# Performance work log

Measured on AMD Instinct MI355X. Metric: run time of the kernel, lower is better.

Reference implementation:

```python
import jax, jax.numpy as jnp
import numpy as np

N = 65536          # nodes
E = N * 7          # edges (avg_degree = n_edge_type = 7)
C_IN = 128
C_OUT = 128
N_EDGE_TYPE = 7
N_NODE_TYPE = 5
FEAT = C_IN + N_NODE_TYPE  # 133, channels after one-hot concat


def setup_inputs() -> dict:
    key = jax.random.key(0)
    k1, k2, k3, k4, k5 = jax.random.split(key, 5)
    x = jax.random.normal(k1, (N, C_IN), dtype=jnp.float32)
    edge_idx = jax.random.randint(k2, (2, E), 0, N, dtype=jnp.int64)
    edge_type = jax.random.randint(k3, (E,), 0, N_EDGE_TYPE, dtype=jnp.int64)
    node_type = jax.random.randint(k4, (N,), 0, N_NODE_TYPE, dtype=jnp.int64)
    # uniform init a la module's reset_parameters
    fan_in = 7 * C_IN
    fan_out = 7 * C_OUT
    a = np.sqrt(3.0) * np.sqrt(2.0 / (fan_in + fan_out))
    weights = jax.random.uniform(k5, (N_EDGE_TYPE * FEAT, C_OUT), dtype=jnp.float32,
                                 minval=-a, maxval=a)
    return {"x": x, "edge_idx": edge_idx, "edge_type": edge_type,
            "node_type": node_type, "weights": weights}


def reference(x, edge_idx, edge_type, node_type, weights):
    # one-hot node type concat (n_node_type > 1 branch)
    one_hot = jax.nn.one_hot(node_type, N_NODE_TYPE, dtype=x.dtype)
    xa = jnp.concatenate([x, one_hot], axis=1)          # [N, FEAT]
    row, col = edge_idx[0], edge_idx[1]
    seg = row * N_EDGE_TYPE + edge_type                 # [E]
    gathered = xa[col]                                  # [E, FEAT]
    num_seg = N * N_EDGE_TYPE
    sums = jax.ops.segment_sum(gathered, seg, num_segments=num_seg)
    cnt = jax.ops.segment_sum(jnp.ones((E,), dtype=xa.dtype), seg, num_segments=num_seg)
    col_data = sums / jnp.maximum(cnt, 1.0)[:, None]    # scatter_mean
    # overwrite self-loop slot (last edge type) with node's own features
    self_idx = jnp.arange(N, dtype=jnp.int64) * N_EDGE_TYPE + (N_EDGE_TYPE - 1)
    col_data = col_data.at[self_idx].set(xa)
    out = col_data.reshape(N, N_EDGE_TYPE * FEAT) @ weights  # [N, C_OUT]
    return out
```

## Files before the change

### kernel.cpp

```cpp
#include <hip/hip_runtime.h>
#include <hip/hip_bf16.h>

#define N_NODES 65536
#define N_EDGES (N_NODES * 7)
#define NSEG    (N_NODES * 7)
#define CAP     12
#define ZROW    65536

typedef short short8 __attribute__((ext_vector_type(8)));
typedef float f32x4  __attribute__((ext_vector_type(4)));

__device__ __forceinline__ unsigned short f2bf(float f) {
    return __builtin_bit_cast(unsigned short, (__bf16)f);
}
__device__ __forceinline__ unsigned pack2(float lo, float hi) {
    return (unsigned)f2bf(lo) | ((unsigned)f2bf(hi) << 16);
}
__device__ __forceinline__ float bflo(unsigned d) { return __uint_as_float(d << 16); }
__device__ __forceinline__ float bfhi(unsigned d) { return __uint_as_float(d & 0xffff0000u); }

__global__ __launch_bounds__(256) void k_big(const float* __restrict__ x,
                                             const int* __restrict__ eidx,
                                             const int* __restrict__ etype,
                                             const int* __restrict__ ntype,
                                             const float* __restrict__ W,
                                             unsigned short* __restrict__ xb,
                                             unsigned short* __restrict__ wb,
                                             unsigned* __restrict__ seg32,
                                             unsigned short* __restrict__ scol) {
    int i = blockIdx.x * 256 + threadIdx.x;

    if (i < N_EDGES) {
        int t = etype[i];
        if (t < 6) {
            int r = eidx[i];
            int c = eidx[N_EDGES + i];
            int u = ntype[c];
            unsigned seg = (unsigned)r * 7u + (unsigned)t;
            unsigned inc = 1u | (1u << (7 + 5 * u));
            unsigned old = atomicAdd(&seg32[seg], inc);
            unsigned slot = old & 0x7fu;
            if (slot < CAP) scol[seg * CAP + slot] = (unsigned short)c;
        }
    }

    {
        int row = i >> 4, mm = i & 15;
        const f32x4* p = reinterpret_cast<const f32x4*>(x + (size_t)row * 128 + mm * 8);
        f32x4 v0 = p[0], v1 = p[1];
        uint4 w;
        w.x = pack2(v0[0], v0[1]); w.y = pack2(v0[2], v0[3]);
        w.z = pack2(v1[0], v1[1]); w.w = pack2(v1[2], v1[3]);
        reinterpret_cast<uint4*>(xb)[i] = w;
    }

    if (i < 16) reinterpret_cast<uint4*>(xb + (size_t)ZROW * 128)[i] = (uint4){0u, 0u, 0u, 0u};

    if (i < 143360) {
        int j    = i & 7;
        int lane = (i >> 3) & 63;
        int cb   = (i >> 9) & 7;
        int tkc  = i >> 12;
        int kc   = tkc % 5;
        int t    = tkc / 5;
        int k = kc * 32 + ((lane >> 4) << 3) + j;
        int c = cb * 16 + (lane & 15);
        float v = (k < 133) ? W[(t * 133 + k) * 128 + c] : 0.0f;
        wb[i] = f2bf(v);
    }
}

__global__ __launch_bounds__(512, 4) void k_main(const unsigned short* __restrict__ xb,
                                                 const int* __restrict__ ntype,
                                                 const unsigned* __restrict__ seg32,
                                                 const unsigned short* __restrict__ scol,
                                                 const unsigned short* __restrict__ wb,
                                                 float* __restrict__ out) {
    __shared__ unsigned short sA[7 * 32 * 168];

    const int tid  = threadIdx.x;
    const int lane = tid & 63;
    const int wid  = tid >> 6;
    const int n0   = blockIdx.x * 32;
    const int r    = tid >> 4;
    const int m    = tid & 15;
    const int n    = n0 + r;

    for (int i = tid; i < 7 * 32 * 12; i += 512) {
        int row = i / 12, j = i - row * 12;
        reinterpret_cast<unsigned*>(sA)[row * 84 + 68 + j] = 0u;
    }

    unsigned sv[6], c_t[6];
    uint2 q2[6];
    #pragma unroll
    for (int t = 0; t < 6; ++t) {
        sv[t]  = seg32[n * 7 + t];
        c_t[t] = sv[t] & 0x7fu;
        q2[t]  = *reinterpret_cast<const uint2*>(scol + ((size_t)n * 7 + t) * CAP);
    }

    short8 xA[6], xB[6], xS;
    #pragma unroll
    for (int t = 0; t < 6; ++t) {
        unsigned cA = (c_t[t] >= 1u) ? (q2[t].x & 0xffffu) : (unsigned)ZROW;
        unsigned cB = (c_t[t] >= 2u) ? (q2[t].x >> 16)     : (unsigned)ZROW;
        xA[t] = *reinterpret_cast<const short8*>(xb + (size_t)cA * 128 + m * 8);
        xB[t] = *reinterpret_cast<const short8*>(xb + (size_t)cB * 128 + m * 8);
    }
    xS = *reinterpret_cast<const short8*>(xb + (size_t)n * 128 + m * 8);
    const int ntS = ntype[n];

    #pragma unroll
    for (int t = 0; t < 6; ++t) {
        const unsigned cntv = c_t[t];
        const float inv = (cntv > 1u) ? __builtin_amdgcn_rcpf((float)cntv) : 1.0f;

        uint4 a4 = *reinterpret_cast<const uint4*>(&xA[t]);
        uint4 b4 = *reinterpret_cast<const uint4*>(&xB[t]);
        float a[8];
        a[0] = bflo(a4.x) + bflo(b4.x); a[1] = bfhi(a4.x) + bfhi(b4.x);
        a[2] = bflo(a4.y) + bflo(b4.y); a[3] = bfhi(a4.y) + bfhi(b4.y);
        a[4] = bflo(a4.z) + bflo(b4.z); a[5] = bfhi(a4.z) + bfhi(b4.z);
        a[6] = bflo(a4.w) + bflo(b4.w); a[7] = bfhi(a4.w) + bfhi(b4.w);

        if (cntv >= 3u) {
            const unsigned ce = (cntv < (unsigned)CAP) ? cntv : (unsigned)CAP;
            {
                unsigned c2 = q2[t].y & 0xffffu;
                short8 v = *reinterpret_cast<const short8*>(xb + (size_t)c2 * 128 + m * 8);
                uint4 v4 = *reinterpret_cast<const uint4*>(&v);
                a[0] += bflo(v4.x); a[1] += bfhi(v4.x);
                a[2] += bflo(v4.y); a[3] += bfhi(v4.y);
                a[4] += bflo(v4.z); a[5] += bfhi(v4.z);
                a[6] += bflo(v4.w); a[7] += bfhi(v4.w);
            }
            if (ce >= 4u) {
                unsigned c3 = q2[t].y >> 16;
                short8 v = *reinterpret_cast<const short8*>(xb + (size_t)c3 * 128 + m * 8);
                uint4 v4 = *reinterpret_cast<const uint4*>(&v);
                a[0] += bflo(v4.x); a[1] += bfhi(v4.x);
                a[2] += bflo(v4.y); a[3] += bfhi(v4.y);
                a[4] += bflo(v4.z); a[5] += bfhi(v4.z);
                a[6] += bflo(v4.w); a[7] += bfhi(v4.w);
                const size_t segbase = ((size_t)n * 7 + t) * CAP;
                for (unsigned e = 4; e < ce; ++e) {
                    unsigned c = scol[segbase + e];
                    short8 ve = *reinterpret_cast<const short8*>(xb + (size_t)c * 128 + m * 8);
                    uint4 v4e = *reinterpret_cast<const uint4*>(&ve);
                    a[0] += bflo(v4e.x); a[1] += bfhi(v4e.x);
                    a[2] += bflo(v4e.y); a[3] += bfhi(v4e.y);
                    a[4] += bflo(v4e.z); a[5] += bfhi(v4e.z);
                    a[6] += bflo(v4e.w); a[7] += bfhi(v4e.w);
                }
            }
        }

        uint4 w;
        w.x = pack2(a[0] * inv, a[1] * inv); w.y = pack2(a[2] * inv, a[3] * inv);
        w.z = pack2(a[4] * inv, a[5] * inv); w.w = pack2(a[6] * inv, a[7] * inv);
        *reinterpret_cast<uint4*>(sA + (t * 32 + r) * 168 + m * 8) = w;

        if (m < 4) {
            int i0 = 2 * m, i1 = 2 * m + 1;
            float g0 = (i0 < 5) ? (float)((sv[t] >> (7 + 5 * i0)) & 31u) : 0.f;
            float g1 = (i1 < 5) ? (float)((sv[t] >> (7 + 5 * i1)) & 31u) : 0.f;
            reinterpret_cast<unsigned*>(sA)[(t * 32 + r) * 84 + 64 + m] =
                pack2(g0 * inv, g1 * inv);
        }
    }

    *reinterpret_cast<uint4*>(sA + (6 * 32 + r) * 168 + m * 8) =
        *reinterpret_cast<const uint4*>(&xS);
    if (m < 4) {
        float g0 = (ntS == 2 * m) ? 1.f : 0.f;
        float g1 = (ntS == 2 * m + 1) ? 1.f : 0.f;
        reinterpret_cast<unsigned*>(sA)[(6 * 32 + r) * 84 + 64 + m] = pack2(g0, g1);
    }

    short8 bv[2][5];
    #pragma unroll
    for (int kc = 0; kc < 5; ++kc)
        bv[0][kc] = *reinterpret_cast<const short8*>(
            wb + (((kc * 8 + wid) << 6) + lane) * 8);

    __syncthreads();

    f32x4 acc0 = {0.f, 0.f, 0.f, 0.f};
    f32x4 acc1 = {0.f, 0.f, 0.f, 0.f};
    const int ar = lane & 15;
    const int hi = (lane >> 4) << 3;

    #pragma unroll
    for (int t = 0; t < 7; ++t) {
        const int cur = t & 1, nxt = cur ^ 1;
        if (t < 6) {
            #pragma unroll
            for (int kc = 0; kc < 5; ++kc)
                bv[nxt][kc] = *reinterpret_cast<const short8*>(
                    wb + (((((t + 1) * 5 + kc) * 8 + wid) << 6) + lane) * 8);
        }
        #pragma unroll
        for (int kc = 0; kc < 5; ++kc) {
            short8 a0 = *reinterpret_cast<const short8*>(
                sA + (t * 32 + ar) * 168 + kc * 32 + hi);
            short8 a1 = *reinterpret_cast<const short8*>(
                sA + (t * 32 + 16 + ar) * 168 + kc * 32 + hi);
            acc0 = __builtin_amdgcn_mfma_f32_16x16x32_bf16(a0, bv[cur][kc], acc0, 0, 0, 0);
            acc1 = __builtin_amdgcn_mfma_f32_16x16x32_bf16(a1, bv[cur][kc], acc1, 0, 0, 0);
        }
    }

    const int orow = n0 + ((lane >> 4) << 2);
    const int ocol = (wid << 4) + (lane & 15);
    #pragma unroll
    for (int rr = 0; rr < 4; ++rr) {
        out[(size_t)(orow + rr) * 128 + ocol]      = acc0[rr];
        out[(size_t)(orow + 16 + rr) * 128 + ocol] = acc1[rr];
    }
}


extern "C" void kernel_launch(void* const* d_in, const int* in_sizes, int n_in,
                              void* d_out, int out_size, void* d_ws, size_t ws_size,
                              hipStream_t stream) {
    const float* x     = (const float*)d_in[0];
    const int*   eidx  = (const int*)d_in[1];
    const int*   etype = (const int*)d_in[2];
    const int*   ntype = (const int*)d_in[3];
    const float* W     = (const float*)d_in[4];
    float* out = (float*)d_out;

    unsigned short* xb    = (unsigned short*)d_ws;
    unsigned short* wb    = (unsigned short*)((char*)d_ws + 16777472);
    unsigned*       seg32 = (unsigned*)((char*)d_ws + 17064192);
    unsigned short* scol  = (unsigned short*)((char*)d_ws + 18899200);

    hipMemsetAsync(seg32, 0, NSEG * sizeof(unsigned), stream);
    k_big <<<4096,         256, 0, stream>>>(x, eidx, etype, ntype, W, xb, wb, seg32, scol);
    k_main<<<N_NODES / 32, 512, 0, stream>>>(xb, ntype, seg32, scol, wb, out);
}
```

Before: 81.44 us.

## Replace LDS-staged 8-wave block with single-wave 32x32 MFMA fused gather-GEMM

The main kernel changes from a 512-thread block that gathers neighbour means into shared memory and then runs 16x16x32 MFMAs to a single 64-lane wave per 32 nodes. That wave gathers its A fragments straight into registers and feeds them to 32x32x16 MFMAs over all 128 output columns, and the weight pre-pack layout is changed to match. This removes the shared memory, the barrier and the LDS round trip. In exchange each wave loops serially over edge types and streams the full weight matrix, so occupancy and latency hiding per CU drop and weight traffic per block grows.

```diff
diff --git a/kernel.cpp b/kernel.cpp
--- a/kernel.cpp
+++ b/kernel.cpp
@@ -9,6 +9,7 @@
 
 typedef short short8 __attribute__((ext_vector_type(8)));
 typedef float f32x4  __attribute__((ext_vector_type(4)));
+typedef float f32x16 __attribute__((ext_vector_type(16)));
 
 __device__ __forceinline__ unsigned short f2bf(float f) {
     return __builtin_bit_cast(unsigned short, (__bf16)f);
@@ -56,167 +57,133 @@
 
     if (i < 16) reinterpret_cast<uint4*>(xb + (size_t)ZROW * 128)[i] = (uint4){0u, 0u, 0u, 0u};
 
-    if (i < 143360) {
+    if (i < 129024) {
         int j    = i & 7;
         int lane = (i >> 3) & 63;
-        int cb   = (i >> 9) & 7;
-        int tkc  = i >> 12;
-        int kc   = tkc % 5;
-        int t    = tkc / 5;
-        int k = kc * 32 + ((lane >> 4) << 3) + j;
-        int c = cb * 16 + (lane & 15);
+        int cg   = (i >> 9) & 3;
+        int tkc  = i >> 11;
+        int kc   = tkc % 9;
+        int t    = tkc / 9;
+        int k = kc * 16 + ((lane >> 5) << 3) + j;
+        int c = (cg << 5) + (lane & 31);
         float v = (k < 133) ? W[(t * 133 + k) * 128 + c] : 0.0f;
         wb[i] = f2bf(v);
     }
 }
 
-__global__ __launch_bounds__(512, 4) void k_main(const unsigned short* __restrict__ xb,
-                                                 const int* __restrict__ ntype,
-                                                 const unsigned* __restrict__ seg32,
-                                                 const unsigned short* __restrict__ scol,
-                                                 const unsigned short* __restrict__ wb,
-                                                 float* __restrict__ out) {
-    __shared__ unsigned short sA[7 * 32 * 168];
-
-    const int tid  = threadIdx.x;
-    const int lane = tid & 63;
-    const int wid  = tid >> 6;
+__global__ __launch_bounds__(64, 4) void k_main(const unsigned short* __restrict__ xb,
+                                                const int* __restrict__ ntype,
+                                                const unsigned* __restrict__ seg32,
+                                                const unsigned short* __restrict__ scol,
+                                                const unsigned short* __restrict__ wb,
+                                                float* __restrict__ out) {
+    const int lane = threadIdx.x;
+    const int r    = lane & 31;
+    const int h    = lane >> 5;
     const int n0   = blockIdx.x * 32;
-    const int r    = tid >> 4;
-    const int m    = tid & 15;
     const int n    = n0 + r;
-
-    for (int i = tid; i < 7 * 32 * 12; i += 512) {
-        int row = i / 12, j = i - row * 12;
-        reinterpret_cast<unsigned*>(sA)[row * 84 + 68 + j] = 0u;
-    }
-
-    unsigned sv[6], c_t[6];
-    uint2 q2[6];
+    const int choff = h * 8;
+
+    const int ntS = ntype[n];
+
+    f32x16 acc[4];
     #pragma unroll
-    for (int t = 0; t < 6; ++t) {
-        sv[t]  = seg32[n * 7 + t];
-        c_t[t] = sv[t] & 0x7fu;
-        q2[t]  = *reinterpret_cast<const uint2*>(scol + ((size_t)n * 7 + t) * CAP);
-    }
-
-    short8 xA[6], xB[6], xS;
+    for (int cg = 0; cg < 4; ++cg)
+        #pragma unroll
+        for (int q = 0; q < 16; ++q) acc[cg][q] = 0.f;
+
+    #pragma unroll 1
+    for (int t = 0; t < 7; ++t) {
+        unsigned svt = 0, cnt, cA, cB;
+        uint2 q2t = {0u, 0u};
+        if (t < 6) {
+            svt = seg32[n * 7 + t];
+            cnt = svt & 0x7fu;
+            q2t = *reinterpret_cast<const uint2*>(scol + ((size_t)n * 7 + t) * CAP);
+            cA = (cnt >= 1u) ? (q2t.x & 0xffffu) : (unsigned)ZROW;
+            cB = (cnt >= 2u) ? (q2t.x >> 16)     : (unsigned)ZROW;
+        } else {
+            cnt = 1u; cA = (unsigned)n; cB = (unsigned)ZROW;
+        }
+        const float inv = (cnt > 1u) ? __builtin_amdgcn_rcpf((float)cnt) : 1.0f;
+        const unsigned ce = (cnt < (unsigned)CAP) ? cnt : (unsigned)CAP;
+        const size_t segbase = ((size_t)n * 7 + t) * CAP;
+
+        #pragma unroll
+        for (int kc = 0; kc < 8; ++kc) {
+            uint4 a4 = *reinterpret_cast<const uint4*>(
+                xb + (size_t)cA * 128 + kc * 16 + choff);
+            uint4 w;
+            if (cnt <= 1u) {
+                w = a4;
+            } else {
+                uint4 b4 = *reinterpret_cast<const uint4*>(
+                    xb + (size_t)cB * 128 + kc * 16 + choff);
+                float f[8];
+                f[0] = bflo(a4.x) + bflo(b4.x); f[1] = bfhi(a4.x) + bfhi(b4.x);
+                f[2] = bflo(a4.y) + bflo(b4.y); f[3] = bfhi(a4.y) + bfhi(b4.y);
+                f[4] = bflo(a4.z) + bflo(b4.z); f[5] = bfhi(a4.z) + bfhi(b4.z);
+                f[6] = bflo(a4.w) + bflo(b4.w); f[7] = bfhi(a4.w) + bfhi(b4.w);
+                if (cnt >= 3u) {
+                    for (unsigned e = 2; e < ce; ++e) {
+                        unsigned c = scol[segbase + e];
+                        uint4 v4 = *reinterpret_cast<const uint4*>(
+                            xb + (size_t)c * 128 + kc * 16 + choff);
+                        f[0] += bflo(v4.x); f[1] += bfhi(v4.x);
+                        f[2] += bflo(v4.y); f[3] += bfhi(v4.y);
+                        f[4] += bflo(v4.z); f[5] += bfhi(v4.z);
+                        f[6] += bflo(v4.w); f[7] += bfhi(v4.w);
+                    }
+                }
+                w.x = pack2(f[0] * inv, f[1] * inv);
+                w.y = pack2(f[2] * inv, f[3] * inv);
+                w.z = pack2(f[4] * inv, f[5] * inv);
+                w.w = pack2(f[6] * inv, f[7] * inv);
+            }
+            short8 av = *reinterpret_cast<const short8*>(&w);
+            #pragma unroll
+            for (int cg = 0; cg < 4; ++cg) {
+                short8 bv = *reinterpret_cast<const short8*>(
+                    wb + ((((t * 9 + kc) * 4 + cg) << 6) + lane) * 8);
+                acc[cg] = __builtin_amdgcn_mfma_f32_32x32x16_bf16(av, bv, acc[cg], 0, 0, 0);
+            }
+        }
+
+        {
+            uint4 w = {0u, 0u, 0u, 0u};
+            if (h == 0) {
+                float g0, g1, g2, g3, g4;
+                if (t < 6) {
+                    g0 = (float)((svt >> 7)  & 31u) * inv;
+                    g1 = (float)((svt >> 12) & 31u) * inv;
+                    g2 = (float)((svt >> 17) & 31u) * inv;
+                    g3 = (float)((svt >> 22) & 31u) * inv;
+                    g4 = (float)((svt >> 27) & 31u) * inv;
+                } else {
+                    g0 = (ntS == 0) ? 1.f : 0.f; g1 = (ntS == 1) ? 1.f : 0.f;
+                    g2 = (ntS == 2) ? 1.f : 0.f; g3 = (ntS == 3) ? 1.f : 0.f;
+                    g4 = (ntS == 4) ? 1.f : 0.f;
+                }
+                w.x = pack2(g0, g1); w.y = pack2(g2, g3); w.z = pack2(g4, 0.f);
+            }
+            short8 av = *reinterpret_cast<const short8*>(&w);
+            #pragma unroll
+            for (int cg = 0; cg < 4; ++cg) {
+                short8 bv = *reinterpret_cast<const short8*>(
+                    wb + ((((t * 9 + 8) * 4 + cg) << 6) + lane) * 8);
+                acc[cg] = __builtin_amdgcn_mfma_f32_32x32x16_bf16(av, bv, acc[cg], 0, 0, 0);
+            }
+        }
+    }
+
+    const int col = lane & 31;
     #pragma unroll
-    for (int t = 0; t < 6; ++t) {
-        unsigned cA = (c_t[t] >= 1u) ? (q2[t].x & 0xffffu) : (unsigned)ZROW;
-        unsigned cB = (c_t[t] >= 2u) ? (q2[t].x >> 16)     : (unsigned)ZROW;
-        xA[t] = *reinterpret_cast<const short8*>(xb + (size_t)cA * 128 + m * 8);
-        xB[t] = *reinterpret_cast<const short8*>(xb + (size_t)cB * 128 + m * 8);
-    }
-    xS = *reinterpret_cast<const short8*>(xb + (size_t)n * 128 + m * 8);
-    const int ntS = ntype[n];
-
-    #pragma unroll
-    for (int t = 0; t < 6; ++t) {
-        const unsigned cntv = c_t[t];
-        const float inv = (cntv > 1u) ? __builtin_amdgcn_rcpf((float)cntv) : 1.0f;
-
-        uint4 a4 = *reinterpret_cast<const uint4*>(&xA[t]);
-        uint4 b4 = *reinterpret_cast<const uint4*>(&xB[t]);
-        float a[8];
-        a[0] = bflo(a4.x) + bflo(b4.x); a[1] = bfhi(a4.x) + bfhi(b4.x);
-        a[2] = bflo(a4.y) + bflo(b4.y); a[3] = bfhi(a4.y) + bfhi(b4.y);
-        a[4] = bflo(a4.z) + bflo(b4.z); a[5] = bfhi(a4.z) + bfhi(b4.z);
-        a[6] = bflo(a4.w) + bflo(b4.w); a[7] = bfhi(a4.w) + bfhi(b4.w);
-
-        if (cntv >= 3u) {
-            const unsigned ce = (cntv < (unsigned)CAP) ? cntv : (unsigned)CAP;
-            {
-                unsigned c2 = q2[t].y & 0xffffu;
-                short8 v = *reinterpret_cast<const short8*>(xb + (size_t)c2 * 128 + m * 8);
-                uint4 v4 = *reinterpret_cast<const uint4*>(&v);
-                a[0] += bflo(v4.x); a[1] += bfhi(v4.x);
-                a[2] += bflo(v4.y); a[3] += bfhi(v4.y);
-                a[4] += bflo(v4.z); a[5] += bfhi(v4.z);
-                a[6] += bflo(v4.w); a[7] += bfhi(v4.w);
-            }
-            if (ce >= 4u) {
-                unsigned c3 = q2[t].y >> 16;
-                short8 v = *reinterpret_cast<const short8*>(xb + (size_t)c3 * 128 + m * 8);
-                uint4 v4 = *reinterpret_cast<const uint4*>(&v);
-                a[0] += bflo(v4.x); a[1] += bfhi(v4.x);
-                a[2] += bflo(v4.y); a[3] += bfhi(v4.y);
-                a[4] += bflo(v4.z); a[5] += bfhi(v4.z);
-                a[6] += bflo(v4.w); a[7] += bfhi(v4.w);
-                const size_t segbase = ((size_t)n * 7 + t) * CAP;
-                for (unsigned e = 4; e < ce; ++e) {
-                    unsigned c = scol[segbase + e];
-                    short8 ve = *reinterpret_cast<const short8*>(xb + (size_t)c * 128 + m * 8);
-                    uint4 v4e = *reinterpret_cast<const uint4*>(&ve);
-                    a[0] += bflo(v4e.x); a[1] += bfhi(v4e.x);
-                    a[2] += bflo(v4e.y); a[3] += bfhi(v4e.y);
-                    a[4] += bflo(v4e.z); a[5] += bfhi(v4e.z);
-                    a[6] += bflo(v4e.w); a[7] += bfhi(v4e.w);
-                }
-            }
-        }
-
-        uint4 w;
-        w.x = pack2(a[0] * inv, a[1] * inv); w.y = pack2(a[2] * inv, a[3] * inv);
-        w.z = pack2(a[4] * inv, a[5] * inv); w.w = pack2(a[6] * inv, a[7] * inv);
-        *reinterpret_cast<uint4*>(sA + (t * 32 + r) * 168 + m * 8) = w;
-
-        if (m < 4) {
-            int i0 = 2 * m, i1 = 2 * m + 1;
-            float g0 = (i0 < 5) ? (float)((sv[t] >> (7 + 5 * i0)) & 31u) : 0.f;
-            float g1 = (i1 < 5) ? (float)((sv[t] >> (7 + 5 * i1)) & 31u) : 0.f;
-            reinterpret_cast<unsigned*>(sA)[(t * 32 + r) * 84 + 64 + m] =
-                pack2(g0 * inv, g1 * inv);
-        }
-    }
-
-    *reinterpret_cast<uint4*>(sA + (6 * 32 + r) * 168 + m * 8) =
-        *reinterpret_cast<const uint4*>(&xS);
-    if (m < 4) {
-        float g0 = (ntS == 2 * m) ? 1.f : 0.f;
-        float g1 = (ntS == 2 * m + 1) ? 1.f : 0.f;
-        reinterpret_cast<unsigned*>(sA)[(6 * 32 + r) * 84 + 64 + m] = pack2(g0, g1);
-    }
-
-    short8 bv[2][5];
-    #pragma unroll
-    for (int kc = 0; kc < 5; ++kc)
-        bv[0][kc] = *reinterpret_cast<const short8*>(
-            wb + (((kc * 8 + wid) << 6) + lane) * 8);
-
-    __syncthreads();
-
-    f32x4 acc0 = {0.f, 0.f, 0.f, 0.f};
-    f32x4 acc1 = {0.f, 0.f, 0.f, 0.f};
-    const int ar = lane & 15;
-    const int hi = (lane >> 4) << 3;
-
-    #pragma unroll
-    for (int t = 0; t < 7; ++t) {
-        const int cur = t & 1, nxt = cur ^ 1;
-        if (t < 6) {
-            #pragma unroll
-            for (int kc = 0; kc < 5; ++kc)
-                bv[nxt][kc] = *reinterpret_cast<const short8*>(
-                    wb + (((((t + 1) * 5 + kc) * 8 + wid) << 6) + lane) * 8);
-        }
+    for (int cg = 0; cg < 4; ++cg) {
         #pragma unroll
-        for (int kc = 0; kc < 5; ++kc) {
-            short8 a0 = *reinterpret_cast<const short8*>(
-                sA + (t * 32 + ar) * 168 + kc * 32 + hi);
-            short8 a1 = *reinterpret_cast<const short8*>(
-                sA + (t * 32 + 16 + ar) * 168 + kc * 32 + hi);
-            acc0 = __builtin_amdgcn_mfma_f32_16x16x32_bf16(a0, bv[cur][kc], acc0, 0, 0, 0);
-            acc1 = __builtin_amdgcn_mfma_f32_16x16x32_bf16(a1, bv[cur][kc], acc1, 0, 0, 0);
-        }
-    }
-
-    const int orow = n0 + ((lane >> 4) << 2);
-    const int ocol = (wid << 4) + (lane & 15);
-    #pragma unroll
-    for (int rr = 0; rr < 4; ++rr) {
-        out[(size_t)(orow + rr) * 128 + ocol]      = acc0[rr];
-        out[(size_t)(orow + 16 + rr) * 128 + ocol] = acc1[rr];
+        for (int reg = 0; reg < 16; ++reg) {
+            const int row = (reg & 3) + 8 * (reg >> 2) + 4 * h;
+            out[(size_t)(n0 + row) * 128 + (cg << 5) + col] = acc[cg][reg];
+        }
     }
 }
 
@@ -233,10 +200,10 @@
 
     unsigned short* xb    = (unsigned short*)d_ws;
     unsigned short* wb    = (unsigned short*)((char*)d_ws + 16777472);
-    unsigned*       seg32 = (unsigned*)((char*)d_ws + 17064192);
-    unsigned short* scol  = (unsigned short*)((char*)d_ws + 18899200);
+    unsigned*       seg32 = (unsigned*)((char*)d_ws + 17035520);
+    unsigned short* scol  = (unsigned short*)((char*)d_ws + 18870528);
 
     hipMemsetAsync(seg32, 0, NSEG * sizeof(unsigned), stream);
     k_big <<<4096,         256, 0, stream>>>(x, eidx, etype, ntype, W, xb, wb, seg32, scol);
-    k_main<<<N_NODES / 32, 512, 0, stream>>>(xb, ntype, seg32, scol, wb, out);
-}
+    k_main<<<N_NODES / 32,  64, 0, stream>>>(xb, ntype, seg32, scol, wb, out);
+}
```

Result: slower. 133.3 us (+63.7%).

## Load single-neighbor and self rows directly into LDS via global_load_lds with XOR swizzle

Applied to the files above, without the earlier changes.

Splits the shared A tile into a 128-wide feature block and a separate one-hot/count block. Rows whose segment has one neighbor, plus the self row, are copied straight from global memory into LDS with global_load_lds, so they skip registers. Only segments with two or more neighbors are reduced in registers and overwrite the LDS slot. The feature block uses an XOR swizzle in place of padding to avoid bank conflicts. The cost is an extra barrier, redundant loads of the first neighbor row, and more complex indexing that depends on the async LDS copies completing at the barrier.

```diff
diff --git a/kernel.cpp b/kernel.cpp
--- a/kernel.cpp
+++ b/kernel.cpp
@@ -9,6 +9,10 @@
 
 typedef short short8 __attribute__((ext_vector_type(8)));
 typedef float f32x4  __attribute__((ext_vector_type(4)));
+
+#define GLDS(g, l) __builtin_amdgcn_global_load_lds(                        \
+    (const __attribute__((address_space(1))) void*)(g),                    \
+    (__attribute__((address_space(3))) void*)(l), 16, 0, 0)
 
 __device__ __forceinline__ unsigned short f2bf(float f) {
     return __builtin_bit_cast(unsigned short, (__bf16)f);
@@ -76,7 +80,8 @@
                                                  const unsigned short* __restrict__ scol,
                                                  const unsigned short* __restrict__ wb,
                                                  float* __restrict__ out) {
-    __shared__ unsigned short sA[7 * 32 * 168];
+    __shared__ unsigned short sAd[7 * 32 * 128];
+    __shared__ unsigned short oh [7 * 32 * 32];
 
     const int tid  = threadIdx.x;
     const int lane = tid & 63;
@@ -85,111 +90,110 @@
     const int r    = tid >> 4;
     const int m    = tid & 15;
     const int n    = n0 + r;
-
-    for (int i = tid; i < 7 * 32 * 12; i += 512) {
-        int row = i / 12, j = i - row * 12;
-        reinterpret_cast<unsigned*>(sA)[row * 84 + 68 + j] = 0u;
-    }
-
-    unsigned sv[6], c_t[6];
-    uint2 q2[6];
+    const int swz  = r & 7;
+
+    {
+        unsigned* zp = reinterpret_cast<unsigned*>(oh);
+        #pragma unroll
+        for (int i = 0; i < 7; ++i) zp[tid + i * 512] = 0u;
+    }
+
+    unsigned sv[6]; uint2 q2[6];
     #pragma unroll
     for (int t = 0; t < 6; ++t) {
-        sv[t]  = seg32[n * 7 + t];
-        c_t[t] = sv[t] & 0x7fu;
-        q2[t]  = *reinterpret_cast<const uint2*>(scol + ((size_t)n * 7 + t) * CAP);
-    }
-
-    short8 xA[6], xB[6], xS;
+        sv[t] = seg32[n * 7 + t];
+        q2[t] = *reinterpret_cast<const uint2*>(scol + ((size_t)n * 7 + t) * CAP);
+    }
+    const int ntS = ntype[n];
+
+    const int gch = (m ^ swz) << 3;
+    #pragma unroll
+    for (int t = 0; t < 7; ++t) {
+        unsigned c0;
+        if (t < 6) {
+            unsigned cnt = sv[t] & 0x7fu;
+            c0 = (cnt >= 1u) ? (q2[t].x & 0xffffu) : (unsigned)ZROW;
+        } else {
+            c0 = (unsigned)n;
+        }
+        GLDS(xb + (size_t)c0 * 128 + gch, sAd + t * 4096 + wid * 512);
+    }
+
+    uint4 rA[6], rB[6];
     #pragma unroll
     for (int t = 0; t < 6; ++t) {
-        unsigned cA = (c_t[t] >= 1u) ? (q2[t].x & 0xffffu) : (unsigned)ZROW;
-        unsigned cB = (c_t[t] >= 2u) ? (q2[t].x >> 16)     : (unsigned)ZROW;
-        xA[t] = *reinterpret_cast<const short8*>(xb + (size_t)cA * 128 + m * 8);
-        xB[t] = *reinterpret_cast<const short8*>(xb + (size_t)cB * 128 + m * 8);
-    }
-    xS = *reinterpret_cast<const short8*>(xb + (size_t)n * 128 + m * 8);
-    const int ntS = ntype[n];
+        unsigned cnt = sv[t] & 0x7fu;
+        unsigned c0 = (cnt >= 1u) ? (q2[t].x & 0xffffu) : (unsigned)ZROW;
+        unsigned c1 = (cnt >= 2u) ? (q2[t].x >> 16)     : (unsigned)ZROW;
+        rA[t] = *reinterpret_cast<const uint4*>(xb + (size_t)c0 * 128 + m * 8);
+        rB[t] = *reinterpret_cast<const uint4*>(xb + (size_t)c1 * 128 + m * 8);
+    }
+
+    __syncthreads();
 
     #pragma unroll
     for (int t = 0; t < 6; ++t) {
-        const unsigned cntv = c_t[t];
-        const float inv = (cntv > 1u) ? __builtin_amdgcn_rcpf((float)cntv) : 1.0f;
-
-        uint4 a4 = *reinterpret_cast<const uint4*>(&xA[t]);
-        uint4 b4 = *reinterpret_cast<const uint4*>(&xB[t]);
-        float a[8];
-        a[0] = bflo(a4.x) + bflo(b4.x); a[1] = bfhi(a4.x) + bfhi(b4.x);
-        a[2] = bflo(a4.y) + bflo(b4.y); a[3] = bfhi(a4.y) + bfhi(b4.y);
-        a[4] = bflo(a4.z) + bflo(b4.z); a[5] = bfhi(a4.z) + bfhi(b4.z);
-        a[6] = bflo(a4.w) + bflo(b4.w); a[7] = bfhi(a4.w) + bfhi(b4.w);
-
-        if (cntv >= 3u) {
-            const unsigned ce = (cntv < (unsigned)CAP) ? cntv : (unsigned)CAP;
-            {
-                unsigned c2 = q2[t].y & 0xffffu;
-                short8 v = *reinterpret_cast<const short8*>(xb + (size_t)c2 * 128 + m * 8);
-                uint4 v4 = *reinterpret_cast<const uint4*>(&v);
-                a[0] += bflo(v4.x); a[1] += bfhi(v4.x);
-                a[2] += bflo(v4.y); a[3] += bfhi(v4.y);
-                a[4] += bflo(v4.z); a[5] += bfhi(v4.z);
-                a[6] += bflo(v4.w); a[7] += bfhi(v4.w);
+        const unsigned cnt = sv[t] & 0x7fu;
+        const float inv = (cnt > 1u) ? __builtin_amdgcn_rcpf((float)cnt) : 1.0f;
+        if (cnt >= 2u) {
+            uint4 a0 = rA[t], b0 = rB[t];
+            float f[8];
+            f[0] = bflo(a0.x) + bflo(b0.x); f[1] = bfhi(a0.x) + bfhi(b0.x);
+            f[2] = bflo(a0.y) + bflo(b0.y); f[3] = bfhi(a0.y) + bfhi(b0.y);
+            f[4] = bflo(a0.z) + bflo(b0.z); f[5] = bfhi(a0.z) + bfhi(b0.z);
+            f[6] = bflo(a0.w) + bflo(b0.w); f[7] = bfhi(a0.w) + bfhi(b0.w);
+            const unsigned ce = (cnt < (unsigned)CAP) ? cnt : (unsigned)CAP;
+            const size_t segbase = ((size_t)n * 7 + t) * CAP;
+            for (unsigned e = 2; e < ce; ++e) {
+                unsigned c = scol[segbase + e];
+                uint4 v = *reinterpret_cast<const uint4*>(xb + (size_t)c * 128 + m * 8);
+                f[0] += bflo(v.x); f[1] += bfhi(v.x);
+                f[2] += bflo(v.y); f[3] += bfhi(v.y);
+                f[4] += bflo(v.z); f[5] += bfhi(v.z);
+                f[6] += bflo(v.w); f[7] += bfhi(v.w);
             }
-            if (ce >= 4u) {
-                unsigned c3 = q2[t].y >> 16;
-                short8 v = *reinterpret_cast<const short8*>(xb + (size_t)c3 * 128 + m * 8);
-                uint4 v4 = *reinterpret_cast<const uint4*>(&v);
-                a[0] += bflo(v4.x); a[1] += bfhi(v4.x);
-                a[2] += bflo(v4.y); a[3] += bfhi(v4.y);
-                a[4] += bflo(v4.z); a[5] += bfhi(v4.z);
-                a[6] += bflo(v4.w); a[7] += bfhi(v4.w);
-                const size_t segbase = ((size_t)n * 7 + t) * CAP;
-                for (unsigned e = 4; e < ce; ++e) {
-                    unsigned c = scol[segbase + e];
-                    short8 ve = *reinterpret_cast<const short8*>(xb + (size_t)c * 128 + m * 8);
-                    uint4 v4e = *reinterpret_cast<const uint4*>(&ve);
-                    a[0] += bflo(v4e.x); a[1] += bfhi(v4e.x);
-                    a[2] += bflo(v4e.y); a[3] += bfhi(v4e.y);
-                    a[4] += bflo(v4e.z); a[5] += bfhi(v4e.z);
-                    a[6] += bflo(v4e.w); a[7] += bfhi(v4e.w);
-                }
-            }
-        }
-
-        uint4 w;
-        w.x = pack2(a[0] * inv, a[1] * inv); w.y = pack2(a[2] * inv, a[3] * inv);
-        w.z = pack2(a[4] * inv, a[5] * inv); w.w = pack2(a[6] * inv, a[7] * inv);
-        *reinterpret_cast<uint4*>(sA + (t * 32 + r) * 168 + m * 8) = w;
-
-        if (m < 4) {
-            int i0 = 2 * m, i1 = 2 * m + 1;
-            float g0 = (i0 < 5) ? (float)((sv[t] >> (7 + 5 * i0)) & 31u) : 0.f;
-            float g1 = (i1 < 5) ? (float)((sv[t] >> (7 + 5 * i1)) & 31u) : 0.f;
-            reinterpret_cast<unsigned*>(sA)[(t * 32 + r) * 84 + 64 + m] =
-                pack2(g0 * inv, g1 * inv);
-        }
-    }
-
-    *reinterpret_cast<uint4*>(sA + (6 * 32 + r) * 168 + m * 8) =
-        *reinterpret_cast<const uint4*>(&xS);
-    if (m < 4) {
-        float g0 = (ntS == 2 * m) ? 1.f : 0.f;
-        float g1 = (ntS == 2 * m + 1) ? 1.f : 0.f;
-        reinterpret_cast<unsigned*>(sA)[(6 * 32 + r) * 84 + 64 + m] = pack2(g0, g1);
-    }
+            uint4 w;
+            w.x = pack2(f[0] * inv, f[1] * inv);
+            w.y = pack2(f[2] * inv, f[3] * inv);
+            w.z = pack2(f[4] * inv, f[5] * inv);
+            w.w = pack2(f[6] * inv, f[7] * inv);
+            *reinterpret_cast<uint4*>(sAd + (t * 32 + r) * 128 + gch) = w;
+        }
+        if (m == 0) {
+            float g0 = (float)((sv[t] >> 7)  & 31u) * inv;
+            float g1 = (float)((sv[t] >> 12) & 31u) * inv;
+            float g2 = (float)((sv[t] >> 17) & 31u) * inv;
+            float g3 = (float)((sv[t] >> 22) & 31u) * inv;
+            float g4 = (float)((sv[t] >> 27) & 31u) * inv;
+            uint4 wo;
+            wo.x = pack2(g0, g1); wo.y = pack2(g2, g3);
+            wo.z = pack2(g4, 0.f); wo.w = 0u;
+            *reinterpret_cast<uint4*>(oh + (t * 32 + r) * 32) = wo;
+        }
+    }
+    if (m == 0) {
+        uint4 wo;
+        wo.x = pack2((float)(ntS == 0), (float)(ntS == 1));
+        wo.y = pack2((float)(ntS == 2), (float)(ntS == 3));
+        wo.z = pack2((float)(ntS == 4), 0.f);
+        wo.w = 0u;
+        *reinterpret_cast<uint4*>(oh + (6 * 32 + r) * 32) = wo;
+    }
+
+    __syncthreads();
+
+    const int arl = lane & 15;
+    const int g8  = (lane >> 4) << 3;
+    const int sgh = g8 >> 3;
+    const int rs  = arl & 7;
+    f32x4 acc0 = {0.f, 0.f, 0.f, 0.f};
+    f32x4 acc1 = {0.f, 0.f, 0.f, 0.f};
 
     short8 bv[2][5];
     #pragma unroll
     for (int kc = 0; kc < 5; ++kc)
         bv[0][kc] = *reinterpret_cast<const short8*>(
             wb + (((kc * 8 + wid) << 6) + lane) * 8);
-
-    __syncthreads();
-
-    f32x4 acc0 = {0.f, 0.f, 0.f, 0.f};
-    f32x4 acc1 = {0.f, 0.f, 0.f, 0.f};
-    const int ar = lane & 15;
-    const int hi = (lane >> 4) << 3;
 
     #pragma unroll
     for (int t = 0; t < 7; ++t) {
@@ -201,13 +205,22 @@
                     wb + (((((t + 1) * 5 + kc) * 8 + wid) << 6) + lane) * 8);
         }
         #pragma unroll
-        for (int kc = 0; kc < 5; ++kc) {
+        for (int kc = 0; kc < 4; ++kc) {
+            const int so = ((kc * 4 + sgh) ^ rs) << 3;
             short8 a0 = *reinterpret_cast<const short8*>(
-                sA + (t * 32 + ar) * 168 + kc * 32 + hi);
+                sAd + (t * 32 + arl) * 128 + so);
             short8 a1 = *reinterpret_cast<const short8*>(
-                sA + (t * 32 + 16 + ar) * 168 + kc * 32 + hi);
+                sAd + (t * 32 + 16 + arl) * 128 + so);
             acc0 = __builtin_amdgcn_mfma_f32_16x16x32_bf16(a0, bv[cur][kc], acc0, 0, 0, 0);
             acc1 = __builtin_amdgcn_mfma_f32_16x16x32_bf16(a1, bv[cur][kc], acc1, 0, 0, 0);
+        }
+        {
+            short8 a0 = *reinterpret_cast<const short8*>(
+                oh + (t * 32 + arl) * 32 + g8);
+            short8 a1 = *reinterpret_cast<const short8*>(
+                oh + (t * 32 + 16 + arl) * 32 + g8);
+            acc0 = __builtin_amdgcn_mfma_f32_16x16x32_bf16(a0, bv[cur][4], acc0, 0, 0, 0);
+            acc1 = __builtin_amdgcn_mfma_f32_16x16x32_bf16(a1, bv[cur][4], acc1, 0, 0, 0);
         }
     }
 
```

New measurement: 89.10 us. 9.4% more time.
